# Kernel tuning notes

Measured on AMD Instinct MI355X. Metric: run time of the kernel, lower is better.

The kernel has to match this reference:

```python
import jax, jax.numpy as jnp
import numpy as np

HEADS = 8
DH_QK = 32
DH_V = 32
BS = 8          # block_size
HALO = 3
WIN = BS + 2 * HALO  # 14
REL = 2 * WIN - 1    # 27
SCALE = DH_QK ** -0.5


def setup_inputs() -> dict:
    key = jax.random.key(0)
    k1, k2, k3, k4, k5 = jax.random.split(key, 5)
    dim = 256
    dim_out_qk = HEADS * DH_QK  # 256
    dim_out_v = HEADS * DH_V    # 256
    std = dim ** -0.5
    x = jax.random.normal(k1, (4, dim, 128, 128), jnp.float32)
    w_q = jax.random.normal(k2, (dim_out_qk, dim), jnp.float32) * std
    w_kv = jax.random.normal(k3, (dim_out_qk + dim_out_v, dim), jnp.float32) * std
    height_rel = jax.random.normal(k4, (REL, DH_QK), jnp.float32) * SCALE
    width_rel = jax.random.normal(k5, (REL, DH_QK), jnp.float32) * SCALE
    return {"x": x, "w_q": w_q, "w_kv": w_kv, "height_rel": height_rel, "width_rel": width_rel}


def rel_logits_1d(q, rel_k, permute):
    N, H, W, d = q.shape
    rel_size = rel_k.shape[0]
    win = (rel_size + 1) // 2
    x = jnp.einsum('nhwd,rd->nhwr', q, rel_k)
    x = x.reshape(-1, W, rel_size)
    x = jnp.pad(x, ((0, 0), (0, 0), (0, 1))).reshape(x.shape[0], -1)
    x = jnp.pad(x, ((0, 0), (0, rel_size - W)))
    x = x.reshape(-1, W + 1, rel_size)
    x = x[:, :W, win - 1:]
    x = x.reshape(N, H, 1, W, win)
    x = jnp.broadcast_to(x, (N, H, win, W, win))
    return x.transpose(permute)


def pos_embed_rel(q, height_rel, width_rel):
    # q: (BH, nblocks, bs*bs, dh)
    B, BB, HW, dh = q.shape
    qb = q.reshape(-1, BS, BS, dh)
    rel_w = rel_logits_1d(qb, width_rel, (0, 1, 3, 2, 4))
    rel_h = rel_logits_1d(qb.transpose(0, 2, 1, 3), height_rel, (0, 3, 1, 4, 2))
    return (rel_h + rel_w).reshape(B, BB, HW, -1)


def reference(x, w_q, w_kv, height_rel, width_rel):
    B, C, H, W = x.shape
    nh, nw = H // BS, W // BS
    nb = nh * nw
    # 1x1 conv projections as einsum
    q = jnp.einsum('bchw,oc->bohw', x, w_q)
    # (B*heads, nb, bs*bs, dh_qk), queries row-major within block, blocks row-major
    q = q.reshape(B * HEADS, DH_QK, nh, BS, nw, BS).transpose(0, 2, 4, 3, 5, 1)
    q = q.reshape(B * HEADS, nb, BS * BS, DH_QK)
    kv = jnp.einsum('bchw,oc->bohw', x, w_kv)
    kv = jnp.pad(kv, ((0, 0), (0, 0), (HALO, HALO), (HALO, HALO)))
    # halo windows via gather (unfold)
    ih = np.arange(nh)[:, None] * BS + np.arange(WIN)[None, :]
    iw = np.arange(nw)[:, None] * BS + np.arange(WIN)[None, :]
    kv = kv[:, :, ih]
    kv = kv[:, :, :, :, iw]
    kv = kv.transpose(0, 1, 2, 4, 3, 5)
    kv = kv.reshape(B * HEADS, DH_QK + DH_V, nb, WIN * WIN).transpose(0, 2, 3, 1)
    k = kv[..., :DH_QK]
    v = kv[..., DH_QK:]
    attn = jnp.einsum('bnqd,bnkd->bnqk', q, k) * SCALE + pos_embed_rel(q, height_rel, width_rel)
    attn = jax.nn.softmax(attn, axis=-1)
    out = jnp.einsum('bnqk,bnkd->bnqd', attn, v)
    # (BH, nb, HW, dv) -> (B, heads*dv, H, W)
    out = out.transpose(0, 3, 2, 1)  # (BH, dv, HW, nb)
    out = out.reshape(-1, BS, BS, nh, nw).transpose(0, 3, 1, 4, 2)
    out = out.reshape(B, HEADS * DH_V, H, W)
    return out
```

## Files before the change

kernel.cpp:

```cpp
#include <hip/hip_runtime.h>
#include <stdint.h>

#define HEADS 8
#define DH    32
#define BSZ   8
#define HALO  3
#define WIN   14
#define NKEY  196
#define CIN   256
#define IMG   128
#define HWPIX 16384
#define MQKV  768
#define SCALE 0.17677669529663689f

#define KS_STRIDE 36
#define VT_STRIDE 228
#define PQ_STRIDE 112
#define QB_STRIDE 64

typedef short bf16x8 __attribute__((ext_vector_type(8)));
typedef short bf16x4 __attribute__((ext_vector_type(4)));
typedef float f32x4  __attribute__((ext_vector_type(4)));
typedef unsigned short u16x4 __attribute__((ext_vector_type(4)));

#define AS1 __attribute__((address_space(1)))
#define AS3 __attribute__((address_space(3)))

__device__ __forceinline__ void gl_lds16(const void* g, void* l) {
  __builtin_amdgcn_global_load_lds((AS1 const unsigned int*)g,
                                   (AS3 unsigned int*)l, 16, 0, 0);
}

__device__ __forceinline__ float bf2f(unsigned short s){ return __uint_as_float(((unsigned int)s) << 16); }
__device__ __forceinline__ unsigned short f2bf(float f){
  unsigned int u = __float_as_uint(f);
  u += 0x7fffu + ((u >> 16) & 1u);
  return (unsigned short)(u >> 16);
}

__device__ __forceinline__ bf16x8 ld2(const unsigned short* p) {
  bf16x4 a = *(const bf16x4*)p;
  bf16x4 b = *(const bf16x4*)(p + 4);
  bf16x8 r;
  r[0]=a[0]; r[1]=a[1]; r[2]=a[2]; r[3]=a[3];
  r[4]=b[0]; r[5]=b[1]; r[6]=b[2]; r[7]=b[3];
  return r;
}

__device__ __forceinline__ void st_bf4(unsigned short* p, f32x4 c) {
  ushort4 o;
  o.x = f2bf(c[0]); o.y = f2bf(c[1]); o.z = f2bf(c[2]); o.w = f2bf(c[3]);
  *(ushort4*)p = o;
}

__global__ void convw_kernel(const float* __restrict__ wq,
                             const float* __restrict__ wkv,
                             unsigned short* __restrict__ Wb)
{
  int idx = blockIdx.x * 256 + threadIdx.x;
  int m = idx >> 6, c4 = idx & 63;
  int h = m / 96, d = m - h * 96;
  const float* src = (d < 32) ? wq  + (size_t)(h * 32 + d) * CIN
                              : wkv + (size_t)(h * 64 + d - 32) * CIN;
  float4 v = *(const float4*)(src + c4 * 4);
  ushort4 o;
  o.x = f2bf(v.x); o.y = f2bf(v.y); o.z = f2bf(v.z); o.w = f2bf(v.w);
  *(ushort4*)(Wb + (size_t)m * CIN + c4 * 4) = o;
}

__global__ void convrel_kernel(const float* __restrict__ hrel,
                               const float* __restrict__ wrel,
                               unsigned short* __restrict__ relb)
{
  int idx = blockIdx.x * 256 + threadIdx.x;
  int r = idx >> 5, c = idx & 31;
  float v = 0.f;
  if (r < 27) v = hrel[r * 32 + c];
  else if (r >= 32 && r < 59) v = wrel[(r - 32) * 32 + c];
  relb[idx] = f2bf(v);
}

__global__ __launch_bounds__(256)
void convx_kernel(const float* __restrict__ x, unsigned short* __restrict__ xb)
{
  __shared__ unsigned short T[64 * 264];
  const int tid = threadIdx.x;
  const int p0 = blockIdx.x * 64;
  const float* xin = x + (size_t)blockIdx.y * CIN * HWPIX;
  unsigned short* xo = xb + ((size_t)blockIdx.y * HWPIX + p0) * CIN;

  for (int idx = tid; idx < 2048; idx += 256) {
    int cp = idx >> 4, f = idx & 15;
    const float* r0 = xin + (size_t)(2 * cp) * HWPIX + p0 + f * 4;
    float4 a = *(const float4*)r0;
    float4 b = *(const float4*)(r0 + HWPIX);
    unsigned short* tp = T + (4 * f) * 264 + 2 * cp;
    *(unsigned int*)(tp      ) = (unsigned int)f2bf(a.x) | ((unsigned int)f2bf(b.x) << 16);
    *(unsigned int*)(tp + 264) = (unsigned int)f2bf(a.y) | ((unsigned int)f2bf(b.y) << 16);
    *(unsigned int*)(tp + 528) = (unsigned int)f2bf(a.z) | ((unsigned int)f2bf(b.z) << 16);
    *(unsigned int*)(tp + 792) = (unsigned int)f2bf(a.w) | ((unsigned int)f2bf(b.w) << 16);
  }
  __syncthreads();
  for (int idx = tid; idx < 2048; idx += 256) {
    int p = idx >> 5, u = idx & 31;
    *(uint4*)(xo + (size_t)p * CIN + u * 8) = *(const uint4*)(T + p * 264 + u * 8);
  }
}

__global__ __launch_bounds__(256, 3)
void proj_kernel(const unsigned short* __restrict__ xb,
                 const unsigned short* __restrict__ Wb,
                 unsigned short* __restrict__ qkv)
{
  __shared__ unsigned short As[128 * 64];
  __shared__ unsigned short Bs[128 * 64];

  const int tid = threadIdx.x;
  const int w = tid >> 6, lane = tid & 63;
  const int g16 = lane >> 4, l15 = lane & 15;
  const int m0 = blockIdx.x * 128;
  const int bl = blockIdx.y >> 7;
  const int p0 = (blockIdx.y & 127) * 128;
  const int wm = w >> 1, wn = w & 1;
  const unsigned short* xrow = xb + ((size_t)bl * HWPIX + p0) * CIN;

  f32x4 acc[4][4];
  #pragma unroll
  for (int i = 0; i < 4; ++i)
    #pragma unroll
    for (int j = 0; j < 4; ++j) acc[i][j] = (f32x4){0.f,0.f,0.f,0.f};

  for (int kk = 0; kk < 4; ++kk) {
    const int k0 = kk * 64;
    #pragma unroll
    for (int c = 0; c < 4; ++c) {
      int ci = w * 4 + c;
      gl_lds16(Wb   + (size_t)(m0 + ci*8 + (lane>>3)) * CIN + k0 + (lane&7)*8, As + ci*512);
      gl_lds16(xrow + (size_t)(     ci*8 + (lane>>3)) * CIN + k0 + (lane&7)*8, Bs + ci*512);
    }
    __syncthreads();

    #pragma unroll
    for (int kh = 0; kh < 2; ++kh) {
      bf16x8 af[4], bfr[4];
      #pragma unroll
      for (int t = 0; t < 4; ++t) {
        af[t]  = *(const bf16x8*)(As + (wm*64 + t*16 + l15)*64 + kh*32 + g16*8);
        bfr[t] = *(const bf16x8*)(Bs + (wn*64 + t*16 + l15)*64 + kh*32 + g16*8);
      }
      #pragma unroll
      for (int tm = 0; tm < 4; ++tm)
        #pragma unroll
        for (int tn = 0; tn < 4; ++tn)
          acc[tm][tn] = __builtin_amdgcn_mfma_f32_16x16x32_bf16(
                          af[tm], bfr[tn], acc[tm][tn], 0, 0, 0);
    }
    __syncthreads();
  }

  #pragma unroll
  for (int tm = 0; tm < 4; ++tm) {
    int ch = m0 + wm*64 + tm*16 + g16*4;
    #pragma unroll
    for (int tn = 0; tn < 4; ++tn) {
      int pix = p0 + wn*64 + tn*16 + l15;
      st_bf4(qkv + ((size_t)bl * HWPIX + pix) * MQKV + ch, acc[tm][tn]);
    }
  }
}

__global__ __launch_bounds__(256, 3)
void attn_kernel(const unsigned short* __restrict__ qkv,
                 const unsigned short* __restrict__ relb,
                 float* __restrict__ out,
                 int b0)
{
  __shared__ unsigned short Ks[224 * KS_STRIDE];
  __shared__ unsigned short Vt[32 * VT_STRIDE];
  __shared__ unsigned short Pq[64 * PQ_STRIDE];
  __shared__ unsigned short QB[64 * QB_STRIDE];

  const int tid = threadIdx.x;
  const int by = blockIdx.x >> 4, bx = blockIdx.x & 15;
  const int hd = blockIdx.y, bb = blockIdx.z;
  const size_t pixbase = (size_t)bb * HWPIX;

  const int w = tid >> 6, lane = tid & 63;
  const int g16 = lane >> 4, l15 = lane & 15;
  const int q = w * 16 + l15;
  const int qy = q >> 3, qx = q & 7;
  const int gy = by * BSZ + qy, gx = bx * BSZ + qx;
  const int rot = qx * 4;

  bf16x8 qf = *(const bf16x8*)(qkv + (pixbase + (size_t)gy * IMG + gx) * MQKV + hd * 96 + g16 * 8);

  *(uint4*)(Pq + tid * 8) = *(const uint4*)(relb + tid * 8);

  for (int idx = tid; idx < 224 * 8; idx += 256) {
    int key = idx >> 3, part = idx & 7;
    int ky = key >> 4, kx = key & 15;
    int sy = by * BSZ - HALO + ky, sx = bx * BSZ - HALO + kx;
    uint4 val = make_uint4(0,0,0,0);
    if (kx < WIN && (unsigned)sy < (unsigned)IMG && (unsigned)sx < (unsigned)IMG)
      val = *(const uint4*)(qkv + (pixbase + sy * IMG + sx) * MQKV + hd * 96 + 32 + part * 8);
    if (part < 4) {
      unsigned short* kp = Ks + key * KS_STRIDE + part * 8;
      *(unsigned long long*)(kp    ) = (unsigned long long)val.x | ((unsigned long long)val.y << 32);
      *(unsigned long long*)(kp + 4) = (unsigned long long)val.z | ((unsigned long long)val.w << 32);
    } else {
      int dh0 = (part - 4) * 8;
      unsigned int u[4] = {val.x, val.y, val.z, val.w};
      #pragma unroll
      for (int e = 0; e < 4; ++e) {
        Vt[(dh0 + 2*e    ) * VT_STRIDE + key] = (unsigned short)(u[e] & 0xffffu);
        Vt[(dh0 + 2*e + 1) * VT_STRIDE + key] = (unsigned short)(u[e] >> 16);
      }
    }
  }
  __syncthreads();

  {
    const unsigned short* Hb = Pq;
    const unsigned short* Wr = Pq + 1024;
    bf16x8 ah0 = *(const bf16x8*)(Hb + l15 * 32 + g16 * 8);
    bf16x8 ah1 = *(const bf16x8*)(Hb + (16 + l15) * 32 + g16 * 8);
    bf16x8 aw0 = *(const bf16x8*)(Wr + l15 * 32 + g16 * 8);
    bf16x8 aw1 = *(const bf16x8*)(Wr + (16 + l15) * 32 + g16 * 8);
    f32x4 z = (f32x4){0.f,0.f,0.f,0.f};
    f32x4 ch0 = __builtin_amdgcn_mfma_f32_16x16x32_bf16(ah0, qf, z, 0, 0, 0);
    f32x4 ch1 = __builtin_amdgcn_mfma_f32_16x16x32_bf16(ah1, qf, z, 0, 0, 0);
    f32x4 cw0 = __builtin_amdgcn_mfma_f32_16x16x32_bf16(aw0, qf, z, 0, 0, 0);
    f32x4 cw1 = __builtin_amdgcn_mfma_f32_16x16x32_bf16(aw1, qf, z, 0, 0, 0);
    unsigned short* QBq = QB + q * QB_STRIDE;
    st_bf4(QBq +      (( 0 + g16 * 4 + rot) & 31), ch0);
    st_bf4(QBq +      ((16 + g16 * 4 + rot) & 31), ch1);
    st_bf4(QBq + 32 + (( 0 + g16 * 4 + rot) & 31), cw0);
    st_bf4(QBq + 32 + ((16 + g16 * 4 + rot) & 31), cw1);
  }
  __syncthreads();

  const unsigned short* QBq = QB + q * QB_STRIDE;
  unsigned short* Prow = Pq + q * PQ_STRIDE;

  const float LOG2E = 1.4426950408889634f;
  const float SL2E  = SCALE * LOG2E;

  float bw2[4];
  #pragma unroll
  for (int i = 0; i < 4; ++i) {
    int kx = g16 * 4 + i;
    bw2[i] = (kx < WIN) ? bf2f(QBq[32 + ((kx - qx + 13 + rot) & 31)]) * LOG2E : -1e30f;
  }
  const int hbase = 13 - qy + rot;

  float lsum = 0.f;
  f32x4 o0 = (f32x4){0.f,0.f,0.f,0.f}, o1 = (f32x4){0.f,0.f,0.f,0.f};
  const f32x4 z = (f32x4){0.f,0.f,0.f,0.f};

  #pragma unroll
  for (int half = 0; half < 2; ++half) {
    #pragma unroll
    for (int u = 0; u < 7; ++u) {
      const int nt = half * 7 + u;
      bf16x8 kf = ld2(Ks + (nt * 16 + l15) * KS_STRIDE + g16 * 8);
      f32x4 c = __builtin_amdgcn_mfma_f32_16x16x32_bf16(kf, qf, z, 0, 0, 0);
      float bh2 = bf2f(QBq[(nt + hbase) & 31]) * LOG2E;
      float p0 = exp2f(fmaf(c[0], SL2E, bh2 + bw2[0]));
      float p1 = exp2f(fmaf(c[1], SL2E, bh2 + bw2[1]));
      float p2 = exp2f(fmaf(c[2], SL2E, bh2 + bw2[2]));
      float p3 = exp2f(fmaf(c[3], SL2E, bh2 + bw2[3]));
      lsum += (p0 + p1) + (p2 + p3);
      unsigned int plo, phi;
      asm("v_cvt_pk_bf16_f32 %0, %1, %2" : "=v"(plo) : "v"(p0), "v"(p1));
      asm("v_cvt_pk_bf16_f32 %0, %1, %2" : "=v"(phi) : "v"(p2), "v"(p3));
      union { unsigned int u32[2]; u16x4 v; } pk_;
      pk_.u32[0] = plo; pk_.u32[1] = phi;
      *(u16x4*)(Prow + u * 16 + g16 * 4) = pk_.v;
    }
    asm volatile("" ::: "memory");
    #pragma unroll
    for (int cc = 0; cc < 4; ++cc) {
      bf16x8 pf = (bf16x8){0,0,0,0,0,0,0,0};
      const bool masked = (cc == 3);
      if (!masked || g16 < 2)
        pf = *(const bf16x8*)(Prow + cc * 32 + g16 * 8);
      int vcol = half * 112 + cc * 32 + g16 * 8;
      if (masked && g16 >= 2) vcol = 0;
      bf16x8 v0 = ld2(Vt + l15 * VT_STRIDE + vcol);
      bf16x8 v1 = ld2(Vt + (16 + l15) * VT_STRIDE + vcol);
      o0 = __builtin_amdgcn_mfma_f32_16x16x32_bf16(v0, pf, o0, 0, 0, 0);
      o1 = __builtin_amdgcn_mfma_f32_16x16x32_bf16(v1, pf, o1, 0, 0, 0);
    }
  }

  lsum += __shfl_xor(lsum, 16);
  lsum += __shfl_xor(lsum, 32);
  float inv = 1.f / lsum;

  float* ob = out + (((size_t)(b0 + bb) * 256 + hd * DH) * HWPIX) + (size_t)gy * IMG + gx;
  #pragma unroll
  for (int i = 0; i < 4; ++i) {
    int dh0 = g16 * 4 + i;
    ob[(size_t)dh0 * HWPIX]        = o0[i] * inv;
    ob[(size_t)(dh0 + 16) * HWPIX] = o1[i] * inv;
  }
}

extern "C" void kernel_launch(void* const* d_in, const int* in_sizes, int n_in,
                              void* d_out, int out_size, void* d_ws, size_t ws_size,
                              hipStream_t stream)
{
  (void)in_sizes; (void)n_in; (void)out_size;
  const float* x    = (const float*)d_in[0];
  const float* wq   = (const float*)d_in[1];
  const float* wkv  = (const float*)d_in[2];
  const float* hrel = (const float*)d_in[3];
  const float* wrel = (const float*)d_in[4];
  float* out = (float*)d_out;

  const size_t wb_bytes   = (size_t)MQKV * CIN * 2;
  const size_t relb_bytes = 4096;
  const size_t xb_per_b   = (size_t)HWPIX * CIN * 2;
  const size_t qkv_per_b  = (size_t)HWPIX * MQKV * 2;
  const int chunk = (ws_size >= wb_bytes + relb_bytes + 4 * (xb_per_b + qkv_per_b)) ? 4 : 1;

  unsigned short* Wb   = (unsigned short*)d_ws;
  unsigned short* relb = (unsigned short*)((char*)d_ws + wb_bytes);
  unsigned short* xb   = (unsigned short*)((char*)d_ws + wb_bytes + relb_bytes);
  unsigned short* qkv  = (unsigned short*)((char*)d_ws + wb_bytes + relb_bytes
                                           + (size_t)chunk * xb_per_b);

  convw_kernel<<<192, 256, 0, stream>>>(wq, wkv, Wb);
  convrel_kernel<<<8, 256, 0, stream>>>(hrel, wrel, relb);

  for (int b0 = 0; b0 < 4; b0 += chunk) {
    convx_kernel<<<dim3(256, chunk), 256, 0, stream>>>(x + (size_t)b0 * CIN * HWPIX, xb);
    proj_kernel<<<dim3(6, 128 * chunk), 256, 0, stream>>>(xb, Wb, qkv);
    attn_kernel<<<dim3(256, HEADS, chunk), 256, 0, stream>>>(qkv, relb, out, b0);
  }
}
```

Measured before the change: 267.5 us.

## Fuse x bf16 conversion into projection GEMM with LDS-staged coalesced output

Merges the fp32-to-bf16 transpose kernel and the projection GEMM. Each block converts a 64-pixel strip of x (all 256 channels) into shared memory, then loops over all six 128-channel weight tiles. This removes the xb intermediate write and read from global memory. The output tile is staged through shared memory with an XOR swizzle so qkv rows are stored as coalesced 16-byte vectors. In exchange, per-block MFMA tiles shrink to 4x2, the weight tiles are reloaded by every block, and the grid drops to 256 blocks per batch. Shared memory rises to about 50KB per block, which may limit occupancy.

```diff
diff --git a/kernel.cpp b/kernel.cpp
--- a/kernel.cpp
+++ b/kernel.cpp
@@ -18,10 +18,13 @@
 #define PQ_STRIDE 112
 #define QB_STRIDE 64
 
+#define BST_STRIDE 264
+
 typedef short bf16x8 __attribute__((ext_vector_type(8)));
 typedef short bf16x4 __attribute__((ext_vector_type(4)));
 typedef float f32x4  __attribute__((ext_vector_type(4)));
 typedef unsigned short u16x4 __attribute__((ext_vector_type(4)));
+typedef unsigned short u16x8 __attribute__((ext_vector_type(8)));
 
 #define AS1 __attribute__((address_space(1)))
 #define AS3 __attribute__((address_space(3)))
@@ -80,92 +83,99 @@
   relb[idx] = f2bf(v);
 }
 
-__global__ __launch_bounds__(256)
-void convx_kernel(const float* __restrict__ x, unsigned short* __restrict__ xb)
-{
-  __shared__ unsigned short T[64 * 264];
+__global__ __launch_bounds__(256, 3)
+void projx_kernel(const float* __restrict__ x,
+                  const unsigned short* __restrict__ Wb,
+                  unsigned short* __restrict__ qkv)
+{
+  __shared__ unsigned short Bst[64 * BST_STRIDE];
+  __shared__ unsigned short As[128 * 64];
+
   const int tid = threadIdx.x;
+  const int w = tid >> 6, lane = tid & 63;
+  const int g16 = lane >> 4, l15 = lane & 15;
   const int p0 = blockIdx.x * 64;
-  const float* xin = x + (size_t)blockIdx.y * CIN * HWPIX;
-  unsigned short* xo = xb + ((size_t)blockIdx.y * HWPIX + p0) * CIN;
+  const int bl = blockIdx.y;
+  const int wm = w >> 1, wn = w & 1;
+  const float* xin = x + (size_t)bl * CIN * HWPIX;
 
   for (int idx = tid; idx < 2048; idx += 256) {
     int cp = idx >> 4, f = idx & 15;
     const float* r0 = xin + (size_t)(2 * cp) * HWPIX + p0 + f * 4;
     float4 a = *(const float4*)r0;
     float4 b = *(const float4*)(r0 + HWPIX);
-    unsigned short* tp = T + (4 * f) * 264 + 2 * cp;
-    *(unsigned int*)(tp      ) = (unsigned int)f2bf(a.x) | ((unsigned int)f2bf(b.x) << 16);
-    *(unsigned int*)(tp + 264) = (unsigned int)f2bf(a.y) | ((unsigned int)f2bf(b.y) << 16);
-    *(unsigned int*)(tp + 528) = (unsigned int)f2bf(a.z) | ((unsigned int)f2bf(b.z) << 16);
-    *(unsigned int*)(tp + 792) = (unsigned int)f2bf(a.w) | ((unsigned int)f2bf(b.w) << 16);
+    unsigned short* bp = Bst + (f * 4) * BST_STRIDE + cp * 2;
+    ushort2 o0_, o1_, o2_, o3_;
+    o0_.x = f2bf(a.x); o0_.y = f2bf(b.x);
+    o1_.x = f2bf(a.y); o1_.y = f2bf(b.y);
+    o2_.x = f2bf(a.z); o2_.y = f2bf(b.z);
+    o3_.x = f2bf(a.w); o3_.y = f2bf(b.w);
+    *(ushort2*)(bp                 ) = o0_;
+    *(ushort2*)(bp + BST_STRIDE    ) = o1_;
+    *(ushort2*)(bp + BST_STRIDE * 2) = o2_;
+    *(ushort2*)(bp + BST_STRIDE * 3) = o3_;
   }
   __syncthreads();
-  for (int idx = tid; idx < 2048; idx += 256) {
-    int p = idx >> 5, u = idx & 31;
-    *(uint4*)(xo + (size_t)p * CIN + u * 8) = *(const uint4*)(T + p * 264 + u * 8);
-  }
-}
-
-__global__ __launch_bounds__(256, 3)
-void proj_kernel(const unsigned short* __restrict__ xb,
-                 const unsigned short* __restrict__ Wb,
-                 unsigned short* __restrict__ qkv)
-{
-  __shared__ unsigned short As[128 * 64];
-  __shared__ unsigned short Bs[128 * 64];
-
-  const int tid = threadIdx.x;
-  const int w = tid >> 6, lane = tid & 63;
-  const int g16 = lane >> 4, l15 = lane & 15;
-  const int m0 = blockIdx.x * 128;
-  const int bl = blockIdx.y >> 7;
-  const int p0 = (blockIdx.y & 127) * 128;
-  const int wm = w >> 1, wn = w & 1;
-  const unsigned short* xrow = xb + ((size_t)bl * HWPIX + p0) * CIN;
-
-  f32x4 acc[4][4];
-  #pragma unroll
-  for (int i = 0; i < 4; ++i)
+
+  for (int mt = 0; mt < 6; ++mt) {
+    const int m0 = mt * 128;
+
+    f32x4 acc[4][2];
     #pragma unroll
-    for (int j = 0; j < 4; ++j) acc[i][j] = (f32x4){0.f,0.f,0.f,0.f};
-
-  for (int kk = 0; kk < 4; ++kk) {
-    const int k0 = kk * 64;
+    for (int i = 0; i < 4; ++i)
+      #pragma unroll
+      for (int j = 0; j < 2; ++j) acc[i][j] = (f32x4){0.f,0.f,0.f,0.f};
+
+    for (int kk = 0; kk < 4; ++kk) {
+      const int k0 = kk * 64;
+      #pragma unroll
+      for (int c = 0; c < 4; ++c) {
+        int ci = w * 4 + c;
+        gl_lds16(Wb + (size_t)(m0 + ci*8 + (lane>>3)) * CIN + k0 + (lane&7)*8, As + ci*512);
+      }
+      __syncthreads();
+
+      #pragma unroll
+      for (int kh = 0; kh < 2; ++kh) {
+        bf16x8 af[4], bfr[2];
+        #pragma unroll
+        for (int t = 0; t < 4; ++t)
+          af[t] = *(const bf16x8*)(As + (wm*64 + t*16 + l15)*64 + kh*32 + g16*8);
+        #pragma unroll
+        for (int t = 0; t < 2; ++t)
+          bfr[t] = *(const bf16x8*)(Bst + (wn*32 + t*16 + l15)*BST_STRIDE + k0 + kh*32 + g16*8);
+        #pragma unroll
+        for (int tm = 0; tm < 4; ++tm)
+          #pragma unroll
+          for (int tn = 0; tn < 2; ++tn)
+            acc[tm][tn] = __builtin_amdgcn_mfma_f32_16x16x32_bf16(
+                            af[tm], bfr[tn], acc[tm][tn], 0, 0, 0);
+      }
+      __syncthreads();
+    }
+
     #pragma unroll
-    for (int c = 0; c < 4; ++c) {
-      int ci = w * 4 + c;
-      gl_lds16(Wb   + (size_t)(m0 + ci*8 + (lane>>3)) * CIN + k0 + (lane&7)*8, As + ci*512);
-      gl_lds16(xrow + (size_t)(     ci*8 + (lane>>3)) * CIN + k0 + (lane&7)*8, Bs + ci*512);
+    for (int tm = 0; tm < 4; ++tm) {
+      int ch = wm*64 + tm*16 + g16*4;
+      #pragma unroll
+      for (int tn = 0; tn < 2; ++tn) {
+        int pix = wn*32 + tn*16 + l15;
+        unsigned int boff = (unsigned)(pix*256 + ((ch*2) ^ ((l15 & 7) << 4)));
+        st_bf4((unsigned short*)((char*)As + boff), acc[tm][tn]);
+      }
     }
     __syncthreads();
-
-    #pragma unroll
-    for (int kh = 0; kh < 2; ++kh) {
-      bf16x8 af[4], bfr[4];
-      #pragma unroll
-      for (int t = 0; t < 4; ++t) {
-        af[t]  = *(const bf16x8*)(As + (wm*64 + t*16 + l15)*64 + kh*32 + g16*8);
-        bfr[t] = *(const bf16x8*)(Bs + (wn*64 + t*16 + l15)*64 + kh*32 + g16*8);
-      }
-      #pragma unroll
-      for (int tm = 0; tm < 4; ++tm)
-        #pragma unroll
-        for (int tn = 0; tn < 4; ++tn)
-          acc[tm][tn] = __builtin_amdgcn_mfma_f32_16x16x32_bf16(
-                          af[tm], bfr[tn], acc[tm][tn], 0, 0, 0);
+    {
+      unsigned short* qrow = qkv + ((size_t)bl * HWPIX + p0) * MQKV + m0;
+      #pragma unroll
+      for (int r = 0; r < 4; ++r) {
+        int pl = w*16 + r*4 + g16;
+        unsigned int boff = (unsigned)(pl*256 + ((l15*16) ^ ((pl & 7) << 4)));
+        u16x8 vv = *(const u16x8*)((const char*)As + boff);
+        *(u16x8*)(qrow + (size_t)pl * MQKV + l15*8) = vv;
+      }
     }
     __syncthreads();
-  }
-
-  #pragma unroll
-  for (int tm = 0; tm < 4; ++tm) {
-    int ch = m0 + wm*64 + tm*16 + g16*4;
-    #pragma unroll
-    for (int tn = 0; tn < 4; ++tn) {
-      int pix = p0 + wn*64 + tn*16 + l15;
-      st_bf4(qkv + ((size_t)bl * HWPIX + pix) * MQKV + ch, acc[tm][tn]);
-    }
   }
 }
 
@@ -320,22 +330,18 @@
 
   const size_t wb_bytes   = (size_t)MQKV * CIN * 2;
   const size_t relb_bytes = 4096;
-  const size_t xb_per_b   = (size_t)HWPIX * CIN * 2;
   const size_t qkv_per_b  = (size_t)HWPIX * MQKV * 2;
-  const int chunk = (ws_size >= wb_bytes + relb_bytes + 4 * (xb_per_b + qkv_per_b)) ? 4 : 1;
+  const int chunk = (ws_size >= wb_bytes + relb_bytes + 4 * qkv_per_b) ? 4 : 1;
 
   unsigned short* Wb   = (unsigned short*)d_ws;
   unsigned short* relb = (unsigned short*)((char*)d_ws + wb_bytes);
-  unsigned short* xb   = (unsigned short*)((char*)d_ws + wb_bytes + relb_bytes);
-  unsigned short* qkv  = (unsigned short*)((char*)d_ws + wb_bytes + relb_bytes
-                                           + (size_t)chunk * xb_per_b);
+  unsigned short* qkv  = (unsigned short*)((char*)d_ws + wb_bytes + relb_bytes);
 
   convw_kernel<<<192, 256, 0, stream>>>(wq, wkv, Wb);
   convrel_kernel<<<8, 256, 0, stream>>>(hrel, wrel, relb);
 
   for (int b0 = 0; b0 < 4; b0 += chunk) {
-    convx_kernel<<<dim3(256, chunk), 256, 0, stream>>>(x + (size_t)b0 * CIN * HWPIX, xb);
-    proj_kernel<<<dim3(6, 128 * chunk), 256, 0, stream>>>(xb, Wb, qkv);
+    projx_kernel<<<dim3(256, chunk), 256, 0, stream>>>(x + (size_t)b0 * CIN * HWPIX, Wb, qkv);
     attn_kernel<<<dim3(256, HEADS, chunk), 256, 0, stream>>>(qkv, relb, out, b0);
   }
 }
```

Result: faster. 257.8 us (-3.6%).
